# Kernel optimization log

Measured on AMD Instinct MI355X. Metric: run time of the kernel, lower is better.

## Reference

```python
import jax, jax.numpy as jnp
import numpy as np
import math

DIM = 256; SEQ = 2048; BSZ = 32; NI = 128; NS = 4; ITERS = 3

def _ln(x, g, b):
    m = x.mean(-1, keepdims=True)
    v = ((x - m) ** 2).mean(-1, keepdims=True)
    return (x - m) / jnp.sqrt(v + 1e-5) * g + b

def _norm(x):
    # torch F.normalize: x / ||x||.clamp_min(1e-12)
    return x / jnp.clip(jnp.linalg.norm(x, axis=-1, keepdims=True), 1e-12, None)

def setup_inputs() -> dict:
    key = jax.random.key(0)
    ks = jax.random.split(key, 16)
    def w(k, shape, s=0.02):
        return jax.random.normal(k, shape, jnp.float32) * s
    return {
        'tokens': jax.random.normal(ks[0], (BSZ, SEQ, DIM), jnp.float32),
        'cls_embed': jax.random.normal(ks[1], (BSZ, DIM), jnp.float32),
        'intent_queries': jax.random.normal(ks[2], (NI, DIM), jnp.float32),
        'noise': jax.random.normal(ks[3], (NI, BSZ, NS, DIM), jnp.float32),
        'Wk': w(ks[4], (DIM, DIM)), 'bk': jnp.zeros(DIM, jnp.float32),
        'Wv': w(ks[5], (DIM, DIM)), 'bv': jnp.zeros(DIM, jnp.float32),
        'Wqs': w(ks[6], (DIM, DIM)), 'bqs': jnp.zeros(DIM, jnp.float32),
        'Wqi': w(ks[7], (DIM, DIM)), 'bqi': jnp.zeros(DIM, jnp.float32),
        'ln1_g': jnp.ones(DIM, jnp.float32), 'ln1_b': jnp.zeros(DIM, jnp.float32),
        'ln2_g': jnp.ones(DIM, jnp.float32), 'ln2_b': jnp.zeros(DIM, jnp.float32),
        'Wf1': w(ks[8], (DIM, 2 * DIM)), 'bf1': jnp.zeros(2 * DIM, jnp.float32),
        'Wf2': w(ks[9], (2 * DIM, DIM)), 'bf2': jnp.zeros(DIM, jnp.float32),
        'slot_mu': w(ks[10], (1, NS, DIM)),  # randn*0.02
        'slot_sigma': jnp.ones((1, NS, DIM), jnp.float32) * 0.1,
        'alpha': jnp.float32(1.0),
        'temperature': jnp.float32(1.0),
    }

def reference(tokens, cls_embed, intent_queries, noise, Wk, bk, Wv, bv,
              Wqs, bqs, Wqi, bqi, ln1_g, ln1_b, ln2_g, ln2_b,
              Wf1, bf1, Wf2, bf2, slot_mu, slot_sigma, alpha, temperature):
    scale = 1.0 / math.sqrt(DIM)
    # k/v are identical across the per-intent loop in the original -> compute once
    k = tokens @ Wk + bk  # [B,S,D]
    v = tokens @ Wv + bv  # [B,S,D]
    cls_n = _norm(cls_embed)  # [B,D]

    def per_intent(q, eps):  # q: [D], eps: [B,NS,D]
        qn = _norm(q)
        q_intent = (q @ Wqi + bqi)[None, None, :]  # broadcast over [B,NS,:]
        slots = slot_mu[0] + eps * slot_sigma[0]   # [B,NS,D]
        for _ in range(ITERS):
            q_slot = slots @ Wqs + bqs + q_intent
            logit = jnp.einsum('bnd,bsd->bns', q_slot, k) * scale
            attn = jax.nn.softmax(logit, axis=-1)
            upd = jnp.einsum('bns,bsd->bnd', attn, v)
            slots = _ln(slots + upd, ln1_g, ln1_b)
            h = _ln(slots, ln2_g, ln2_b)
            slots = slots + jax.nn.gelu(h @ Wf1 + bf1, approximate=False) @ Wf2 + bf2
        sn = _norm(slots)                               # [B,NS,D]
        a = jax.nn.softmax(jnp.einsum('bnd,d->bn', sn, qn), axis=-1)
        summ = jnp.einsum('bn,bnd->bd', a, slots)       # slot_summary
        fused = cls_n + alpha * _norm(summ)
        return fused @ qn                               # [B]

    scores = jax.vmap(per_intent)(intent_queries, noise)  # [NI,B]
    logits = scores.T / jnp.maximum(temperature, 1e-4)    # [B,NI]
    return logits
```

## Files before the change

### kernel.cpp

```cpp
#include <hip/hip_runtime.h>
#include <math.h>

#define BSZ 32
#define NI  128

typedef __attribute__((ext_vector_type(8))) _Float16 f16x8;
typedef __attribute__((ext_vector_type(4))) _Float16 f16x4;
typedef __attribute__((ext_vector_type(4))) float    f32x4;

#define MFMA16(a, b, c) __builtin_amdgcn_mfma_f32_16x16x32_f16((a), (b), (c), 0, 0, 0)

#define GLL(g, l) __builtin_amdgcn_global_load_lds(                          \
    (const __attribute__((address_space(1))) void*)(g),                      \
    (__attribute__((address_space(3))) void*)(l), 16, 0, 0)

#define LGKM_BAR() do {                                                      \
    asm volatile("s_waitcnt lgkmcnt(0)" ::: "memory");                       \
    __builtin_amdgcn_sched_barrier(0);                                       \
    __builtin_amdgcn_s_barrier();                                            \
    __builtin_amdgcn_sched_barrier(0); } while (0)

__device__ inline float dot4f(float4 a, float4 b) {
    return a.x * b.x + a.y * b.y + a.z * b.z + a.w * b.w;
}

__device__ inline float4* slp(float* base, int r, int c) {
    return (float4*)(base + r * 256 + ((((c) >> 2) ^ (r & 7)) << 2));
}

__device__ inline void tpose64(const float* __restrict__ src, int Csrc,
                               _Float16* __restrict__ dstT, int KT,
                               int r0, int c0, _Float16 (*tbuf)[72], int tid)
{
#pragma unroll
    for (int it = 0; it < 4; it++) {
        int idx = tid + it * 256;
        int rr = idx >> 4, c4 = idx & 15;
        float4 w = *(const float4*)(src + (size_t)(r0 + rr) * Csrc + c0 + c4 * 4);
        tbuf[c4 * 4 + 0][rr] = (_Float16)w.x;
        tbuf[c4 * 4 + 1][rr] = (_Float16)w.y;
        tbuf[c4 * 4 + 2][rr] = (_Float16)w.z;
        tbuf[c4 * 4 + 3][rr] = (_Float16)w.w;
    }
    __syncthreads();
#pragma unroll
    for (int it = 0; it < 2; it++) {
        int idx = tid + it * 256;
        int orr = idx >> 3, oc8 = idx & 7;
        int n = c0 + orr;
        size_t tile = (size_t)(n >> 4) * KT + (r0 >> 5) + (oc8 >> 2);
        *(f16x8*)(dstT + tile * 512 + (n & 15) * 32 + (oc8 & 3) * 8) = *(const f16x8*)&tbuf[orr][oc8 * 8];
    }
}

__global__ __launch_bounds__(256) void prep(
    const float* __restrict__ Wk, const float* __restrict__ Wv,
    const float* __restrict__ Wqs, const float* __restrict__ Wf1,
    const float* __restrict__ Wf2,
    const float* __restrict__ intent_q, const float* __restrict__ Wqi,
    const float* __restrict__ bqi, const float* __restrict__ bqs,
    const float* __restrict__ cls_embed,
    _Float16* __restrict__ wkT, _Float16* __restrict__ wvT,
    _Float16* __restrict__ wqsT, _Float16* __restrict__ wf1T,
    _Float16* __restrict__ wf2T,
    float* __restrict__ qint2, float* __restrict__ qn, float* __restrict__ clsn)
{
    __shared__ _Float16 tbuf[64][72];
    __shared__ float buf[256];
    __shared__ float red[4];
    const int t = threadIdx.x, blk = blockIdx.x;
    const int lane = t & 63, w = t >> 6;

    if (blk < 112) {
        if (blk < 16)       tpose64(Wk, 256, wkT, 8, (blk >> 2) * 64, (blk & 3) * 64, tbuf, t);
        else if (blk < 32)  { int tt = blk - 16; tpose64(Wv, 256, wvT, 8, (tt >> 2) * 64, (tt & 3) * 64, tbuf, t); }
        else if (blk < 48)  { int tt = blk - 32; tpose64(Wqs, 256, wqsT, 8, (tt >> 2) * 64, (tt & 3) * 64, tbuf, t); }
        else if (blk < 80)  { int tt = blk - 48; tpose64(Wf1, 512, wf1T, 8, (tt & 3) * 64, (tt >> 2) * 64, tbuf, t); }
        else                { int tt = blk - 80; tpose64(Wf2, 256, wf2T, 16, (tt >> 2) * 64, (tt & 3) * 64, tbuf, t); }
    } else if (blk < 240) {
        int i = blk - 112;
        float x = intent_q[(size_t)i * 256 + t];
        buf[t] = x;
        float ss = x * x;
#pragma unroll
        for (int m = 1; m < 64; m <<= 1) ss += __shfl_xor(ss, m, 64);
        if (lane == 0) red[w] = ss;
        __syncthreads();
        float tot = red[0] + red[1] + red[2] + red[3];
        qn[(size_t)i * 256 + t] = x / fmaxf(sqrtf(tot), 1e-12f);
        float acc = bqi[t] + bqs[t];
        for (int e = 0; e < 256; e += 4) {
            const float4 q4 = *(const float4*)&buf[e];
            acc += q4.x * Wqi[(size_t)(e + 0) * 256 + t];
            acc += q4.y * Wqi[(size_t)(e + 1) * 256 + t];
            acc += q4.z * Wqi[(size_t)(e + 2) * 256 + t];
            acc += q4.w * Wqi[(size_t)(e + 3) * 256 + t];
        }
        qint2[(size_t)i * 256 + t] = acc;
    } else {
        int b = blk - 240;
        float x = cls_embed[(size_t)b * 256 + t];
        float ss = x * x;
#pragma unroll
        for (int m = 1; m < 64; m <<= 1) ss += __shfl_xor(ss, m, 64);
        if (lane == 0) red[w] = ss;
        __syncthreads();
        float tot = red[0] + red[1] + red[2] + red[3];
        clsn[(size_t)b * 256 + t] = x / fmaxf(sqrtf(tot), 1e-12f);
    }
}

__global__ __launch_bounds__(512, 2) void kvf_k(
    const float* __restrict__ tokens,
    const _Float16* __restrict__ wkT, const _Float16* __restrict__ wvT,
    const float* __restrict__ bk, const float* __restrict__ bv,
    _Float16* __restrict__ kT, _Float16* __restrict__ vT)
{
    __shared__ __align__(16) _Float16 Sb[2][8192];

    const int t = threadIdx.x, lane = t & 63, w = t >> 6;
    const int l15 = lane & 15, quad = lane >> 4;
    const int lofs = l15 * 32 + quad * 8;
    const int lofsA = ((l15 * 4 + quad) ^ ((l15 >> 1) & 7)) * 8;
    const int bx = blockIdx.x;
    const int b = bx & 31, chunk = bx >> 5;

    f16x8 wk[2][8], wv[2][8];
#pragma unroll
    for (int j = 0; j < 2; j++)
#pragma unroll
        for (int ks = 0; ks < 8; ks++) {
            wk[j][ks] = *(const f16x8*)(wkT + ((size_t)(2 * w + j) * 8 + ks) * 512 + lofs);
            wv[j][ks] = *(const f16x8*)(wvT + ((size_t)(2 * w + j) * 8 + ks) * 512 + lofs);
        }
    f32x4 bi0 = *(const f32x4*)(bk + w * 32 + quad * 4);
    f32x4 bi1 = *(const f32x4*)(bk + w * 32 + 16 + quad * 4);
    const float bv0 = bv[(2 * w) * 16 + l15];
    const float bv1 = bv[(2 * w + 1) * 16 + l15];

    const int rr = t >> 5, d8 = t & 31;
    const float* tbase = tokens + ((size_t)b * 2048 + chunk * 256) * 256 + rr * 256 + d8 * 8;
    const int mskW = ((rr >> 1) & 7) ^ (((d8 >> 2) & 3) << 1);
    const int wofs0 = (d8 >> 2) * 512 + (((rr * 4 + (d8 & 3)) ^ mskW) * 8);
    const int wofs1 = wofs0 + 8 * 512;

    float4 pa0, pa1, pb0, pb1;

#define KVF_LOADS(P) do {                                                    \
        const float* sp_ = tbase + (size_t)(P) * 8192;                       \
        pa0 = *(const float4*)(sp_);                                         \
        pa1 = *(const float4*)(sp_ + 4);                                     \
        pb0 = *(const float4*)(sp_ + 4096);                                  \
        pb1 = *(const float4*)(sp_ + 4100);                                  \
    } while (0)

#define KVF_STAGE(BUF) do {                                                  \
        f16x8 h0, h1;                                                        \
        h0[0] = (_Float16)pa0.x; h0[1] = (_Float16)pa0.y;                    \
        h0[2] = (_Float16)pa0.z; h0[3] = (_Float16)pa0.w;                    \
        h0[4] = (_Float16)pa1.x; h0[5] = (_Float16)pa1.y;                    \
        h0[6] = (_Float16)pa1.z; h0[7] = (_Float16)pa1.w;                    \
        h1[0] = (_Float16)pb0.x; h1[1] = (_Float16)pb0.y;                    \
        h1[2] = (_Float16)pb0.z; h1[3] = (_Float16)pb0.w;                    \
        h1[4] = (_Float16)pb1.x; h1[5] = (_Float16)pb1.y;                    \
        h1[6] = (_Float16)pb1.z; h1[7] = (_Float16)pb1.w;                    \
        *(f16x8*)((BUF) + wofs0) = h0;                                       \
        *(f16x8*)((BUF) + wofs1) = h1;                                       \
    } while (0)

    KVF_LOADS(0);
    KVF_STAGE(&Sb[0][0]);
    LGKM_BAR();

    for (int p = 0; p < 8; p++) {
        if (p < 7) KVF_LOADS(p + 1);
        __builtin_amdgcn_sched_barrier(0);

        const _Float16* lb = &Sb[p & 1][0];
        const int stg0 = chunk * 16 + p * 2;
        const int sp = chunk * 8 + p;

        f16x8 a[2][8];
#pragma unroll
        for (int st = 0; st < 2; st++)
#pragma unroll
            for (int ks = 0; ks < 8; ks++)
                a[st][ks] = *(const f16x8*)(lb + (st * 8 + ks) * 512 + (lofsA ^ ((ks & 3) * 16)));

#pragma unroll
        for (int st = 0; st < 2; st++) {
            f32x4 c0 = {0.f, 0.f, 0.f, 0.f}, c1 = {0.f, 0.f, 0.f, 0.f};
#pragma unroll
            for (int ks = 0; ks < 8; ks++) {
                c0 = MFMA16(wk[0][ks], a[st][ks], c0);
                c1 = MFMA16(wk[1][ks], a[st][ks], c1);
            }
            f16x4 p0, p1;
#pragma unroll
            for (int reg = 0; reg < 4; reg++) {
                p0[reg] = (_Float16)(c0[reg] + bi0[reg]);
                p1[reg] = (_Float16)(c1[reg] + bi1[reg]);
            }
            _Float16* tp = kT + ((size_t)(b * 128 + stg0 + st) * 8 + w) * 512 + l15 * 32;
            *(f16x4*)(tp + (quad >> 1) * 8 + (quad & 1) * 4) = p0;
            *(f16x4*)(tp + (2 + (quad >> 1)) * 8 + (quad & 1) * 4) = p1;
        }

#pragma unroll
        for (int j = 0; j < 2; j++) {
            f32x4 c0 = {0.f, 0.f, 0.f, 0.f}, c1 = {0.f, 0.f, 0.f, 0.f};
#pragma unroll
            for (int ks = 0; ks < 8; ks++) {
                c0 = MFMA16(a[0][ks], wv[j][ks], c0);
                c1 = MFMA16(a[1][ks], wv[j][ks], c1);
            }
            const float bb = j ? bv1 : bv0;
            f16x4 p0, p1;
#pragma unroll
            for (int reg = 0; reg < 4; reg++) {
                p0[reg] = (_Float16)(c0[reg] + bb);
                p1[reg] = (_Float16)(c1[reg] + bb);
            }
            _Float16* tp = vT + ((size_t)(b * 16 + 2 * w + j) * 64 + sp) * 512 + l15 * 32;
            *(f16x4*)(tp + (quad >> 1) * 8 + (quad & 1) * 4) = p0;
            *(f16x4*)(tp + (2 + (quad >> 1)) * 8 + (quad & 1) * 4) = p1;
        }

        if (p < 7) {
            KVF_STAGE(&Sb[(p + 1) & 1][0]);
            LGKM_BAR();
        }
    }
#undef KVF_LOADS
#undef KVF_STAGE
}

__global__ __launch_bounds__(256) void slots_init(
    const float* __restrict__ noise, const float* __restrict__ slot_mu,
    const float* __restrict__ slot_sigma, float* __restrict__ slots,
    _Float16* __restrict__ slotsT)
{
    int idx = blockIdx.x * 256 + threadIdx.x;
    int row = idx >> 5, d8 = idx & 31;
    int b = row >> 9, i = (row >> 2) & 127, n = row & 3;
    int d = d8 * 8;
    const float* mp = slot_mu + n * 256 + d;
    const float* sp = slot_sigma + n * 256 + d;
    const float* np = noise + (((size_t)i * BSZ + b) * 4 + n) * 256 + d;
    float4 o0, o1;
    {
        float4 mu = *(const float4*)mp, sg = *(const float4*)sp, ns = *(const float4*)np;
        o0.x = mu.x + ns.x * sg.x; o0.y = mu.y + ns.y * sg.y;
        o0.z = mu.z + ns.z * sg.z; o0.w = mu.w + ns.w * sg.w;
    }
    {
        float4 mu = *(const float4*)(mp + 4), sg = *(const float4*)(sp + 4), ns = *(const float4*)(np + 4);
        o1.x = mu.x + ns.x * sg.x; o1.y = mu.y + ns.y * sg.y;
        o1.z = mu.z + ns.z * sg.z; o1.w = mu.w + ns.w * sg.w;
    }
    *(float4*)(slots + (size_t)row * 256 + d) = o0;
    *(float4*)(slots + (size_t)row * 256 + d + 4) = o1;
    f16x8 h;
    h[0] = (_Float16)o0.x; h[1] = (_Float16)o0.y; h[2] = (_Float16)o0.z; h[3] = (_Float16)o0.w;
    h[4] = (_Float16)o1.x; h[5] = (_Float16)o1.y; h[6] = (_Float16)o1.z; h[7] = (_Float16)o1.w;
    *(f16x8*)(slotsT + ((size_t)(row >> 4) * 8 + (d8 >> 2)) * 512 + (row & 15) * 32 + (d8 & 3) * 8) = h;
}

__global__ __launch_bounds__(256) void qslot_k(
    const _Float16* __restrict__ slotsT, const _Float16* __restrict__ wqsT,
    const float* __restrict__ qint2, _Float16* __restrict__ qsT)
{
    const int tid = threadIdx.x, lane = tid & 63, wv = tid >> 6;
    const int l15 = lane & 15, quad = lane >> 4;
    const int lofs = l15 * 32 + quad * 8;
    const int bx = blockIdx.x, rb = bx >> 2, dq = bx & 3;
    const int rt = rb * 4 + wv;
    const int gr0 = rt * 16;

    f16x8 bs[8];
#pragma unroll
    for (int ks = 0; ks < 8; ks++)
        bs[ks] = *(const f16x8*)(slotsT + ((size_t)rt * 8 + ks) * 512 + lofs);
    const int iq = ((gr0 + l15) & 511) >> 2;
#pragma unroll
    for (int dt = 0; dt < 4; dt++) {
        int dti = dq * 4 + dt;
        f32x4 c = {0.f, 0.f, 0.f, 0.f};
#pragma unroll
        for (int ks = 0; ks < 8; ks++)
            c = MFMA16(*(const f16x8*)(wqsT + ((size_t)dti * 8 + ks) * 512 + lofs), bs[ks], c);
        float4 qi = *(const float4*)(qint2 + (size_t)iq * 256 + dti * 16 + quad * 4);
        f16x4 o;
#pragma unroll
        for (int reg = 0; reg < 4; reg++) o[reg] = (_Float16)((c[reg] + qi[reg]) * 0.0625f);
        *(f16x4*)(qsT + ((size_t)rt * 8 + (dti >> 1)) * 512 + l15 * 32
                  + ((dti & 1) * 2 + (quad >> 1)) * 8 + (quad & 1) * 4) = o;
    }
}

__global__ __launch_bounds__(512, 2) void attn_k(
    const _Float16* __restrict__ qsT, const _Float16* __restrict__ kT,
    const _Float16* __restrict__ vT,
    _Float16* __restrict__ Opart, float* __restrict__ psum4)
{
    __shared__ __align__(16) _Float16 Kb[2][16384];
    __shared__ __align__(16) _Float16 Vb[16384];
    __shared__ __align__(16) _Float16 pb[8][2304];

    const int tid = threadIdx.x, lane = tid & 63, wv = tid >> 6;
    const int l15 = lane & 15, quad = lane >> 4;
    const int lofs = l15 * 32 + quad * 8;
    const int lofsA = ((l15 * 4 + quad) ^ ((l15 >> 1) & 7)) * 8;
    const int lnsw = (lane ^ ((lane >> 3) & 7)) * 8;
    const int bx = blockIdx.x;
    const int b = bx & 31, rb = (bx >> 5) & 1, sk = bx >> 6;
    const int gr0 = b * 512 + rb * 256 + wv * 32;
    const int rt_q = gr0 >> 4;

    _Float16* pw = pb[wv];

    const _Float16* kSrc = kT + ((size_t)(b * 128 + sk * 32) * 8) * 512;

    {
        const _Float16* src = kSrc + (size_t)(wv * 4) * 512 + lnsw;
        _Float16* dst = &Kb[0][(wv * 4) * 512 + lane * 8];
#pragma unroll
        for (int j = 0; j < 4; j++) GLL(src + j * 512, dst + j * 512);
    }

    f16x8 q[2][8];
#pragma unroll
    for (int m = 0; m < 2; m++)
#pragma unroll
        for (int ks = 0; ks < 8; ks++)
            q[m][ks] = *(const f16x8*)(qsT + ((size_t)(rt_q + m) * 8 + ks) * 512 + lofs);

    f32x4 O[2][16];
#pragma unroll
    for (int m = 0; m < 2; m++)
#pragma unroll
        for (int dt = 0; dt < 16; dt++) O[m][dt] = (f32x4){0.f, 0.f, 0.f, 0.f};
    float ps[2][4] = {{0.f, 0.f, 0.f, 0.f}, {0.f, 0.f, 0.f, 0.f}};

    asm volatile("s_waitcnt vmcnt(0)" ::: "memory");
    __builtin_amdgcn_s_barrier();
    __builtin_amdgcn_sched_barrier(0);

    for (int s = 0; s < 8; s++) {
        const int cur = s & 1;

        {
            const int seg0 = wv * 4;
#pragma unroll
            for (int j = 0; j < 4; j++) {
                const int seg = seg0 + j;
                const _Float16* src = vT
                    + ((size_t)(b * 16 + (seg >> 1)) * 64 + sk * 16 + s * 2 + (seg & 1)) * 512
                    + lnsw;
                GLL(src, &Vb[seg * 512 + lane * 8]);
            }
        }
        if (s < 7) {
            const _Float16* src = kSrc + (size_t)(s + 1) * 16384 + (wv * 4) * 512 + lnsw;
            _Float16* dst = &Kb[cur ^ 1][(wv * 4) * 512 + lane * 8];
#pragma unroll
            for (int j = 0; j < 4; j++) GLL(src + j * 512, dst + j * 512);
            asm volatile("s_waitcnt vmcnt(8)" ::: "memory");
        } else {
            asm volatile("s_waitcnt vmcnt(4)" ::: "memory");
        }
        __builtin_amdgcn_s_barrier();
        __builtin_amdgcn_sched_barrier(0);

#pragma unroll
        for (int kt = 0; kt < 4; kt++) {
            const _Float16* kp = &Kb[cur][(kt * 8) * 512];
            f32x4 c0 = {0.f, 0.f, 0.f, 0.f}, c1 = {0.f, 0.f, 0.f, 0.f};
#pragma unroll
            for (int ks = 0; ks < 8; ks++) {
                f16x8 kf = *(const f16x8*)(kp + ks * 512 + lofsA);
                c0 = MFMA16(q[0][ks], kf, c0);
                c1 = MFMA16(q[1][ks], kf, c1);
            }
            const int col = kt * 16 + l15;
#pragma unroll
            for (int reg = 0; reg < 4; reg++) {
                float p0 = __expf(fminf(c0[reg], 10.5f));
                float p1 = __expf(fminf(c1[reg], 10.5f));
                ps[0][reg] += p0;
                ps[1][reg] += p1;
                pw[(quad * 4 + reg) * 72 + col] = (_Float16)p0;
                pw[(16 + quad * 4 + reg) * 72 + col] = (_Float16)p1;
            }
        }

        __builtin_amdgcn_sched_barrier(0);
        if (s < 7) {
            asm volatile("s_waitcnt vmcnt(4)" ::: "memory");
        } else {
            asm volatile("s_waitcnt vmcnt(0)" ::: "memory");
        }
        __builtin_amdgcn_s_barrier();
        __builtin_amdgcn_sched_barrier(0);

        f16x8 pa[2][2];
#pragma unroll
        for (int m = 0; m < 2; m++)
#pragma unroll
            for (int kg = 0; kg < 2; kg++)
                pa[m][kg] = *(const f16x8*)(pw + (m * 16 + l15) * 72 + kg * 32 + quad * 8);
#pragma unroll
        for (int dt = 0; dt < 16; dt++) {
            const _Float16* vp = &Vb[dt * 1024];
            f16x8 v0 = *(const f16x8*)(vp + lofsA);
            f16x8 v1 = *(const f16x8*)(vp + 512 + lofsA);
            O[0][dt] = MFMA16(pa[0][0], v0, O[0][dt]);
            O[0][dt] = MFMA16(pa[0][1], v1, O[0][dt]);
            O[1][dt] = MFMA16(pa[1][0], v0, O[1][dt]);
            O[1][dt] = MFMA16(pa[1][1], v1, O[1][dt]);
        }

        __builtin_amdgcn_sched_barrier(0);
        __builtin_amdgcn_s_barrier();
        __builtin_amdgcn_sched_barrier(0);
    }

#pragma unroll
    for (int m = 0; m < 2; m++) {
#pragma unroll
        for (int msk = 1; msk <= 8; msk <<= 1)
#pragma unroll
            for (int reg = 0; reg < 4; reg++) ps[m][reg] += __shfl_xor(ps[m][reg], msk, 64);
        if (l15 == 0) {
#pragma unroll
            for (int reg = 0; reg < 4; reg++)
                psum4[(size_t)sk * 16384 + gr0 + m * 16 + quad * 4 + reg] = ps[m][reg];
        }
    }

#pragma unroll
    for (int m = 0; m < 2; m++) {
#pragma unroll
        for (int hd = 0; hd < 2; hd++) {
#pragma unroll
            for (int dt = 0; dt < 8; dt++) {
                const int dti = hd * 8 + dt;
#pragma unroll
                for (int reg = 0; reg < 4; reg++)
                    pw[(quad * 4 + reg) * 136 + dt * 16 + l15] = (_Float16)O[m][dti][reg];
            }
#pragma unroll
            for (int p2 = 0; p2 < 4; p2++) {
                const int u = lane + p2 * 64;
                const int row = u >> 4, col8 = u & 15;
                *(f16x8*)(Opart + ((size_t)sk * 16384 + gr0 + m * 16 + row) * 256 + hd * 128 + col8 * 8) =
                    *(const f16x8*)(pw + row * 136 + col8 * 8);
            }
        }
    }
}

__global__ __launch_bounds__(256, 2) void mlp_k(
    const _Float16* __restrict__ Opart, const float* __restrict__ psum4,
    float* __restrict__ slots,
    const float* __restrict__ ln1_g, const float* __restrict__ ln1_b,
    const float* __restrict__ ln2_g, const float* __restrict__ ln2_b,
    const _Float16* __restrict__ wf1T, const float* __restrict__ bf1,
    const _Float16* __restrict__ wf2T, const float* __restrict__ bf2,
    const _Float16* __restrict__ wqsT, const float* __restrict__ qint2,
    _Float16* __restrict__ qsT,
    const float* __restrict__ qn, const float* __restrict__ clsn,
    const float* __restrict__ alphap, const float* __restrict__ tempp,
    float* __restrict__ out, int it)
{
    __shared__ float sl[32 * 256];
    __shared__ float2 st2[32];
    __shared__ __align__(16) _Float16 actL[16384];

    const int tid = threadIdx.x, lane = tid & 63, w4 = tid >> 6;
    const int l15 = lane & 15, quad = lane >> 4;
    const int lofs = l15 * 32 + quad * 8;
    const int lofsA = ((l15 * 4 + quad) ^ ((l15 >> 1) & 7)) * 8;
    const int pairW = w4 >> 1, half = w4 & 1;
    const int bx = blockIdx.x;
    const int b = bx & 31, rg = bx >> 5;
    const int R0 = b * 512 + rg * 32;

#pragma unroll
    for (int r2 = 0; r2 < 2; r2++) {
        const int lr = w4 * 8 + r2 * 4 + quad;
        const int gr = R0 + lr;
        float l = 0.f;
#pragma unroll
        for (int j = 0; j < 4; j++) l += psum4[(size_t)j * 16384 + gr];
        const float invl = 1.f / l;
        float4 y[4];
        float sm = 0.f, sq = 0.f;
#pragma unroll
        for (int k = 0; k < 4; k++) {
            const int c = k * 64 + l15 * 4;
            float4 o4 = {0.f, 0.f, 0.f, 0.f};
#pragma unroll
            for (int j = 0; j < 4; j++) {
                f16x4 p = *(const f16x4*)(Opart + ((size_t)j * 16384 + gr) * 256 + c);
                o4.x += (float)p[0]; o4.y += (float)p[1];
                o4.z += (float)p[2]; o4.w += (float)p[3];
            }
            float4 s4 = *(const float4*)(slots + (size_t)gr * 256 + c);
            y[k].x = s4.x + o4.x * invl; y[k].y = s4.y + o4.y * invl;
            y[k].z = s4.z + o4.z * invl; y[k].w = s4.w + o4.w * invl;
            sm += y[k].x + y[k].y + y[k].z + y[k].w;
            sq += dot4f(y[k], y[k]);
        }
#pragma unroll
        for (int m = 1; m <= 8; m <<= 1) { sm += __shfl_xor(sm, m, 64); sq += __shfl_xor(sq, m, 64); }
        const float mean = sm * (1.f / 256.f);
        const float rstd = rsqrtf(sq * (1.f / 256.f) - mean * mean + 1e-5f);
        float sm2 = 0.f, sq2 = 0.f;
#pragma unroll
        for (int k = 0; k < 4; k++) {
            const int c = k * 64 + l15 * 4;
            float4 g1 = *(const float4*)(ln1_g + c);
            float4 b1 = *(const float4*)(ln1_b + c);
            float4 x1;
            x1.x = (y[k].x - mean) * rstd * g1.x + b1.x;
            x1.y = (y[k].y - mean) * rstd * g1.y + b1.y;
            x1.z = (y[k].z - mean) * rstd * g1.z + b1.z;
            x1.w = (y[k].w - mean) * rstd * g1.w + b1.w;
            *slp(sl, lr, c) = x1;
            sm2 += x1.x + x1.y + x1.z + x1.w;
            sq2 += dot4f(x1, x1);
        }
#pragma unroll
        for (int m = 1; m <= 8; m <<= 1) { sm2 += __shfl_xor(sm2, m, 64); sq2 += __shfl_xor(sq2, m, 64); }
        const float mean2 = sm2 * (1.f / 256.f);
        const float rstd2 = rsqrtf(sq2 * (1.f / 256.f) - mean2 * mean2 + 1e-5f);
        if (l15 == 0) st2[lr] = make_float2(mean2, rstd2);
    }
    __syncthreads();

    const int lrf = pairW * 16 + l15;
    {
        const float2 s2 = st2[lrf];
        f16x8 bh[8];
#pragma unroll
        for (int ks = 0; ks < 8; ks++) {
            const int c0 = ks * 32 + quad * 8;
            float4 xa = *slp(sl, lrf, c0);
            float4 xb = *slp(sl, lrf, c0 + 4);
            float4 ga = *(const float4*)(ln2_g + c0);
            float4 gb = *(const float4*)(ln2_g + c0 + 4);
            float4 ba = *(const float4*)(ln2_b + c0);
            float4 bb2 = *(const float4*)(ln2_b + c0 + 4);
            bh[ks][0] = (_Float16)((xa.x - s2.x) * s2.y * ga.x + ba.x);
            bh[ks][1] = (_Float16)((xa.y - s2.x) * s2.y * ga.y + ba.y);
            bh[ks][2] = (_Float16)((xa.z - s2.x) * s2.y * ga.z + ba.z);
            bh[ks][3] = (_Float16)((xa.w - s2.x) * s2.y * ga.w + ba.w);
            bh[ks][4] = (_Float16)((xb.x - s2.x) * s2.y * gb.x + bb2.x);
            bh[ks][5] = (_Float16)((xb.y - s2.x) * s2.y * gb.y + bb2.y);
            bh[ks][6] = (_Float16)((xb.z - s2.x) * s2.y * gb.z + bb2.z);
            bh[ks][7] = (_Float16)((xb.w - s2.x) * s2.y * gb.w + bb2.w);
        }
#pragma unroll 2
        for (int t16 = 0; t16 < 16; t16++) {
            const int hti = half * 16 + t16;
            f32x4 c = {0.f, 0.f, 0.f, 0.f};
#pragma unroll
            for (int ks = 0; ks < 8; ks++)
                c = MFMA16(*(const f16x8*)(wf1T + ((size_t)hti * 8 + ks) * 512 + lofs), bh[ks], c);
            float4 bb = *(const float4*)(bf1 + hti * 16 + quad * 4);
            f16x4 o;
#pragma unroll
            for (int reg = 0; reg < 4; reg++) {
                float xg = c[reg] + bb[reg];
                o[reg] = (_Float16)(0.5f * xg * (1.f + erff(xg * 0.70710678118654752f)));
            }
            const int gA = l15 * 4 + (hti & 1) * 2 + (quad >> 1);
            *(f16x4*)(actL + ((size_t)(pairW * 16 + (hti >> 1))) * 512
                      + ((gA ^ ((l15 >> 1) & 7)) * 8) + (quad & 1) * 4) = o;
        }
    }
    __syncthreads();

    {
        f32x4 c[8];
#pragma unroll
        for (int d = 0; d < 8; d++) {
            const int dti = half * 8 + d;
            float4 x4 = *slp(sl, lrf, dti * 16 + quad * 4);
            float4 bb = *(const float4*)(bf2 + dti * 16 + quad * 4);
            c[d] = (f32x4){x4.x + bb.x, x4.y + bb.y, x4.z + bb.z, x4.w + bb.w};
        }
        const _Float16* ap = actL + ((size_t)pairW * 16) * 512;
        for (int ks = 0; ks < 16; ks++) {
            f16x8 afrag = *(const f16x8*)(ap + (size_t)ks * 512 + lofsA);
#pragma unroll
            for (int d = 0; d < 8; d++)
                c[d] = MFMA16(*(const f16x8*)(wf2T + ((size_t)(half * 8 + d) * 16 + ks) * 512 + lofs),
                              afrag, c[d]);
        }
#pragma unroll
        for (int d = 0; d < 8; d++) {
            const int dti = half * 8 + d;
            float4 v = {c[d][0], c[d][1], c[d][2], c[d][3]};
            *slp(sl, lrf, dti * 16 + quad * 4) = v;
        }
    }
    __syncthreads();

    if (it < 2) {
        f16x8 bs[8];
#pragma unroll
        for (int ks = 0; ks < 8; ks++) {
            const int c0 = ks * 32 + quad * 8;
            float4 xa = *slp(sl, lrf, c0);
            float4 xb = *slp(sl, lrf, c0 + 4);
            bs[ks][0] = (_Float16)xa.x; bs[ks][1] = (_Float16)xa.y;
            bs[ks][2] = (_Float16)xa.z; bs[ks][3] = (_Float16)xa.w;
            bs[ks][4] = (_Float16)xb.x; bs[ks][5] = (_Float16)xb.y;
            bs[ks][6] = (_Float16)xb.z; bs[ks][7] = (_Float16)xb.w;
        }
        const int iq = (rg * 32 + pairW * 16 + l15) >> 2;
        const int rtg = b * 32 + rg * 2 + pairW;
#pragma unroll
        for (int d = 0; d < 8; d++) {
            const int dti = half * 8 + d;
            f32x4 c = {0.f, 0.f, 0.f, 0.f};
#pragma unroll
            for (int ks = 0; ks < 8; ks++)
                c = MFMA16(*(const f16x8*)(wqsT + ((size_t)dti * 8 + ks) * 512 + lofs), bs[ks], c);
            float4 qi = *(const float4*)(qint2 + (size_t)iq * 256 + dti * 16 + quad * 4);
            f16x4 o;
#pragma unroll
            for (int reg = 0; reg < 4; reg++) o[reg] = (_Float16)((c[reg] + qi[reg]) * 0.0625f);
            *(f16x4*)(qsT + ((size_t)rtg * 8 + (dti >> 1)) * 512 + l15 * 32
                      + ((dti & 1) * 2 + (quad >> 1)) * 8 + (quad & 1) * 4) = o;
        }
        {
            const int lr2 = tid >> 3, k8 = tid & 7;
#pragma unroll
            for (int q4 = 0; q4 < 8; q4++) {
                float4 v = *slp(sl, lr2, k8 * 32 + q4 * 4);
                *(float4*)(slots + (size_t)(R0 + lr2) * 256 + k8 * 32 + q4 * 4) = v;
            }
        }
    } else {
#pragma unroll
        for (int ii = 0; ii < 2; ii++) {
            const int i_loc = w4 * 2 + ii;
            const int i = rg * 8 + i_loc;
            float4 qv = *(const float4*)(qn + (size_t)i * 256 + lane * 4);
            float4 xs[4];
            float st4[4];
#pragma unroll
            for (int n = 0; n < 4; n++) {
                xs[n] = *slp(sl, i_loc * 4 + n, lane * 4);
                float ss = dot4f(xs[n], xs[n]);
                float sq = dot4f(xs[n], qv);
#pragma unroll
                for (int m = 1; m < 64; m <<= 1) { ss += __shfl_xor(ss, m, 64); sq += __shfl_xor(sq, m, 64); }
                st4[n] = sq / fmaxf(sqrtf(ss), 1e-12f);
            }
            float mx = fmaxf(fmaxf(st4[0], st4[1]), fmaxf(st4[2], st4[3]));
            float e0 = __expf(st4[0] - mx), e1 = __expf(st4[1] - mx);
            float e2 = __expf(st4[2] - mx), e3 = __expf(st4[3] - mx);
            float inv = 1.f / (e0 + e1 + e2 + e3);
            float4 smv;
            smv.x = (e0 * xs[0].x + e1 * xs[1].x + e2 * xs[2].x + e3 * xs[3].x) * inv;
            smv.y = (e0 * xs[0].y + e1 * xs[1].y + e2 * xs[2].y + e3 * xs[3].y) * inv;
            smv.z = (e0 * xs[0].z + e1 * xs[1].z + e2 * xs[2].z + e3 * xs[3].z) * inv;
            smv.w = (e0 * xs[0].w + e1 * xs[1].w + e2 * xs[2].w + e3 * xs[3].w) * inv;
            float ssm = dot4f(smv, smv);
            float sqn = dot4f(smv, qv);
            float4 cv = *(const float4*)(clsn + (size_t)b * 256 + lane * 4);
            float cq = dot4f(cv, qv);
#pragma unroll
            for (int m = 1; m < 64; m <<= 1) {
                ssm += __shfl_xor(ssm, m, 64);
                sqn += __shfl_xor(sqn, m, 64);
                cq  += __shfl_xor(cq,  m, 64);
            }
            if (lane == 0) {
                float score = cq + alphap[0] * sqn / fmaxf(sqrtf(ssm), 1e-12f);
                out[(size_t)b * NI + i] = score / fmaxf(tempp[0], 1e-4f);
            }
        }
    }
}

extern "C" void kernel_launch(void* const* d_in, const int* in_sizes, int n_in,
                              void* d_out, int out_size, void* d_ws, size_t ws_size,
                              hipStream_t stream)
{
    const float* tokens     = (const float*)d_in[0];
    const float* cls_embed  = (const float*)d_in[1];
    const float* intent_q   = (const float*)d_in[2];
    const float* noise      = (const float*)d_in[3];
    const float* Wk  = (const float*)d_in[4];
    const float* bk  = (const float*)d_in[5];
    const float* Wv  = (const float*)d_in[6];
    const float* bv  = (const float*)d_in[7];
    const float* Wqs = (const float*)d_in[8];
    const float* bqs = (const float*)d_in[9];
    const float* Wqi = (const float*)d_in[10];
    const float* bqi = (const float*)d_in[11];
    const float* ln1g = (const float*)d_in[12];
    const float* ln1b = (const float*)d_in[13];
    const float* ln2g = (const float*)d_in[14];
    const float* ln2b = (const float*)d_in[15];
    const float* Wf1 = (const float*)d_in[16];
    const float* bf1 = (const float*)d_in[17];
    const float* Wf2 = (const float*)d_in[18];
    const float* bf2 = (const float*)d_in[19];
    const float* slot_mu    = (const float*)d_in[20];
    const float* slot_sigma = (const float*)d_in[21];
    const float* alphap = (const float*)d_in[22];
    const float* tempp  = (const float*)d_in[23];
    float* out = (float*)d_out;

    char* base = (char*)d_ws;
    _Float16* qsT   = (_Float16*)(base);
    _Float16* slotsT= (_Float16*)(base + 8388608u);
    _Float16* kT    = (_Float16*)(base + 33554432u);
    _Float16* vT    = (_Float16*)(base + 67108864u);
    _Float16* Opart = (_Float16*)(base + 100663296u);
    float* slots    = (float*)(base + 134217728u);
    _Float16* wkT   = (_Float16*)(base + 150994944u);
    _Float16* wvT   = (_Float16*)(base + 151126016u);
    _Float16* wqsT  = (_Float16*)(base + 151257088u);
    _Float16* wf1T  = (_Float16*)(base + 151388160u);
    _Float16* wf2T  = (_Float16*)(base + 151650304u);
    float* qint2    = (float*)(base + 151912448u);
    float* qnb      = (float*)(base + 152043520u);
    float* clsn     = (float*)(base + 152174592u);
    float* psum4    = (float*)(base + 152207360u);

    prep<<<272, 256, 0, stream>>>(Wk, Wv, Wqs, Wf1, Wf2, intent_q, Wqi, bqi, bqs,
                                  cls_embed, wkT, wvT, wqsT, wf1T, wf2T,
                                  qint2, qnb, clsn);
    kvf_k<<<256, 512, 0, stream>>>(tokens, wkT, wvT, bk, bv, kT, vT);
    slots_init<<<2048, 256, 0, stream>>>(noise, slot_mu, slot_sigma, slots, slotsT);
    qslot_k<<<1024, 256, 0, stream>>>(slotsT, wqsT, qint2, qsT);

    for (int it = 0; it < 3; it++) {
        attn_k<<<256, 512, 0, stream>>>(qsT, kT, vT, Opart, psum4);
        mlp_k<<<512, 256, 0, stream>>>(Opart, psum4, slots,
                                       ln1g, ln1b, ln2g, ln2b,
                                       wf1T, bf1, wf2T, bf2,
                                       wqsT, qint2, qsT,
                                       qnb, clsn, alphap, tempp, out, it);
    }
}
```

Measured before the change: 490.0 us.

## Fuse slot init with q-slot projection and halve mlp_k rows per block

Merges slots_init and qslot_k into one kernel that builds the slot rows in shared memory and projects them with Wqs directly, which drops the fp16 slotsT round trip and one launch. mlp_k now handles 16 rows per block instead of 32, with the grid doubled to 1024 and occupancy raised to 4 blocks per CU. Shared memory per block is halved and each wave covers a quarter of the output columns instead of pairs of waves splitting the work. Each block now reloads the Wf1/Wf2/Wqs weight fragments for fewer rows, so weight traffic per row goes up. An extra barrier guards the in-place writes to shared memory.

Measured after the change: 473.6 us. -3.3%, faster.

```diff
diff --git a/kernel.cpp b/kernel.cpp
--- a/kernel.cpp
+++ b/kernel.cpp
@@ -235,56 +235,54 @@
 #undef KVF_STAGE
 }
 
-__global__ __launch_bounds__(256) void slots_init(
+__global__ __launch_bounds__(256, 4) void slotq_k(
     const float* __restrict__ noise, const float* __restrict__ slot_mu,
-    const float* __restrict__ slot_sigma, float* __restrict__ slots,
-    _Float16* __restrict__ slotsT)
+    const float* __restrict__ slot_sigma,
+    const _Float16* __restrict__ wqsT, const float* __restrict__ qint2,
+    float* __restrict__ slots, _Float16* __restrict__ qsT)
 {
-    int idx = blockIdx.x * 256 + threadIdx.x;
-    int row = idx >> 5, d8 = idx & 31;
-    int b = row >> 9, i = (row >> 2) & 127, n = row & 3;
-    int d = d8 * 8;
-    const float* mp = slot_mu + n * 256 + d;
-    const float* sp = slot_sigma + n * 256 + d;
-    const float* np = noise + (((size_t)i * BSZ + b) * 4 + n) * 256 + d;
-    float4 o0, o1;
-    {
-        float4 mu = *(const float4*)mp, sg = *(const float4*)sp, ns = *(const float4*)np;
-        o0.x = mu.x + ns.x * sg.x; o0.y = mu.y + ns.y * sg.y;
-        o0.z = mu.z + ns.z * sg.z; o0.w = mu.w + ns.w * sg.w;
-    }
-    {
-        float4 mu = *(const float4*)(mp + 4), sg = *(const float4*)(sp + 4), ns = *(const float4*)(np + 4);
-        o1.x = mu.x + ns.x * sg.x; o1.y = mu.y + ns.y * sg.y;
-        o1.z = mu.z + ns.z * sg.z; o1.w = mu.w + ns.w * sg.w;
-    }
-    *(float4*)(slots + (size_t)row * 256 + d) = o0;
-    *(float4*)(slots + (size_t)row * 256 + d + 4) = o1;
-    f16x8 h;
-    h[0] = (_Float16)o0.x; h[1] = (_Float16)o0.y; h[2] = (_Float16)o0.z; h[3] = (_Float16)o0.w;
-    h[4] = (_Float16)o1.x; h[5] = (_Float16)o1.y; h[6] = (_Float16)o1.z; h[7] = (_Float16)o1.w;
-    *(f16x8*)(slotsT + ((size_t)(row >> 4) * 8 + (d8 >> 2)) * 512 + (row & 15) * 32 + (d8 & 3) * 8) = h;
-}
-
-__global__ __launch_bounds__(256) void qslot_k(
-    const _Float16* __restrict__ slotsT, const _Float16* __restrict__ wqsT,
-    const float* __restrict__ qint2, _Float16* __restrict__ qsT)
-{
-    const int tid = threadIdx.x, lane = tid & 63, wv = tid >> 6;
+    __shared__ float sb[16 * 256];
+    const int tid = threadIdx.x, lane = tid & 63, w4 = tid >> 6;
     const int l15 = lane & 15, quad = lane >> 4;
     const int lofs = l15 * 32 + quad * 8;
-    const int bx = blockIdx.x, rb = bx >> 2, dq = bx & 3;
-    const int rt = rb * 4 + wv;
+    const int rt = blockIdx.x;
     const int gr0 = rt * 16;
 
+    {
+        const int lr = w4 * 4 + quad;
+        const int gr = gr0 + lr;
+        const int b = gr >> 9, i = (gr >> 2) & 127, n = gr & 3;
+        const float* np = noise + (((size_t)i * BSZ + b) * 4 + n) * 256;
+#pragma unroll
+        for (int k = 0; k < 4; k++) {
+            const int c = k * 64 + l15 * 4;
+            float4 mu = *(const float4*)(slot_mu + n * 256 + c);
+            float4 sg = *(const float4*)(slot_sigma + n * 256 + c);
+            float4 ns = *(const float4*)(np + c);
+            float4 o;
+            o.x = mu.x + ns.x * sg.x; o.y = mu.y + ns.y * sg.y;
+            o.z = mu.z + ns.z * sg.z; o.w = mu.w + ns.w * sg.w;
+            *slp(sb, lr, c) = o;
+            *(float4*)(slots + (size_t)gr * 256 + c) = o;
+        }
+    }
+    __syncthreads();
+
     f16x8 bs[8];
 #pragma unroll
-    for (int ks = 0; ks < 8; ks++)
-        bs[ks] = *(const f16x8*)(slotsT + ((size_t)rt * 8 + ks) * 512 + lofs);
+    for (int ks = 0; ks < 8; ks++) {
+        const int c0 = ks * 32 + quad * 8;
+        float4 xa = *slp(sb, l15, c0);
+        float4 xb = *slp(sb, l15, c0 + 4);
+        bs[ks][0] = (_Float16)xa.x; bs[ks][1] = (_Float16)xa.y;
+        bs[ks][2] = (_Float16)xa.z; bs[ks][3] = (_Float16)xa.w;
+        bs[ks][4] = (_Float16)xb.x; bs[ks][5] = (_Float16)xb.y;
+        bs[ks][6] = (_Float16)xb.z; bs[ks][7] = (_Float16)xb.w;
+    }
     const int iq = ((gr0 + l15) & 511) >> 2;
 #pragma unroll
-    for (int dt = 0; dt < 4; dt++) {
-        int dti = dq * 4 + dt;
+    for (int d = 0; d < 4; d++) {
+        const int dti = w4 * 4 + d;
         f32x4 c = {0.f, 0.f, 0.f, 0.f};
 #pragma unroll
         for (int ks = 0; ks < 8; ks++)
@@ -460,7 +458,7 @@
     }
 }
 
-__global__ __launch_bounds__(256, 2) void mlp_k(
+__global__ __launch_bounds__(256, 4) void mlp_k(
     const _Float16* __restrict__ Opart, const float* __restrict__ psum4,
     float* __restrict__ slots,
     const float* __restrict__ ln1_g, const float* __restrict__ ln1_b,
@@ -473,22 +471,20 @@
     const float* __restrict__ alphap, const float* __restrict__ tempp,
     float* __restrict__ out, int it)
 {
-    __shared__ float sl[32 * 256];
-    __shared__ float2 st2[32];
-    __shared__ __align__(16) _Float16 actL[16384];
+    __shared__ float sl[16 * 256];
+    __shared__ float2 st2[16];
+    __shared__ __align__(16) _Float16 actL[8192];
 
     const int tid = threadIdx.x, lane = tid & 63, w4 = tid >> 6;
     const int l15 = lane & 15, quad = lane >> 4;
     const int lofs = l15 * 32 + quad * 8;
     const int lofsA = ((l15 * 4 + quad) ^ ((l15 >> 1) & 7)) * 8;
-    const int pairW = w4 >> 1, half = w4 & 1;
     const int bx = blockIdx.x;
     const int b = bx & 31, rg = bx >> 5;
-    const int R0 = b * 512 + rg * 32;
-
-#pragma unroll
-    for (int r2 = 0; r2 < 2; r2++) {
-        const int lr = w4 * 8 + r2 * 4 + quad;
+    const int R0 = b * 512 + rg * 16;
+
+    {
+        const int lr = w4 * 4 + quad;
         const int gr = R0 + lr;
         float l = 0.f;
 #pragma unroll
@@ -539,15 +535,14 @@
     }
     __syncthreads();
 
-    const int lrf = pairW * 16 + l15;
     {
-        const float2 s2 = st2[lrf];
+        const float2 s2 = st2[l15];
         f16x8 bh[8];
 #pragma unroll
         for (int ks = 0; ks < 8; ks++) {
             const int c0 = ks * 32 + quad * 8;
-            float4 xa = *slp(sl, lrf, c0);
-            float4 xb = *slp(sl, lrf, c0 + 4);
+            float4 xa = *slp(sl, l15, c0);
+            float4 xb = *slp(sl, l15, c0 + 4);
             float4 ga = *(const float4*)(ln2_g + c0);
             float4 gb = *(const float4*)(ln2_g + c0 + 4);
             float4 ba = *(const float4*)(ln2_b + c0);
@@ -562,8 +557,8 @@
             bh[ks][7] = (_Float16)((xb.w - s2.x) * s2.y * gb.w + bb2.w);
         }
 #pragma unroll 2
-        for (int t16 = 0; t16 < 16; t16++) {
-            const int hti = half * 16 + t16;
+        for (int t8 = 0; t8 < 8; t8++) {
+            const int hti = w4 * 8 + t8;
             f32x4 c = {0.f, 0.f, 0.f, 0.f};
 #pragma unroll
             for (int ks = 0; ks < 8; ks++)
@@ -576,34 +571,34 @@
                 o[reg] = (_Float16)(0.5f * xg * (1.f + erff(xg * 0.70710678118654752f)));
             }
             const int gA = l15 * 4 + (hti & 1) * 2 + (quad >> 1);
-            *(f16x4*)(actL + ((size_t)(pairW * 16 + (hti >> 1))) * 512
+            *(f16x4*)(actL + ((size_t)(hti >> 1)) * 512
                       + ((gA ^ ((l15 >> 1) & 7)) * 8) + (quad & 1) * 4) = o;
         }
     }
     __syncthreads();
 
     {
-        f32x4 c[8];
-#pragma unroll
-        for (int d = 0; d < 8; d++) {
-            const int dti = half * 8 + d;
-            float4 x4 = *slp(sl, lrf, dti * 16 + quad * 4);
+        f32x4 c[4];
+#pragma unroll
+        for (int d = 0; d < 4; d++) {
+            const int dti = w4 * 4 + d;
+            float4 x4 = *slp(sl, l15, dti * 16 + quad * 4);
             float4 bb = *(const float4*)(bf2 + dti * 16 + quad * 4);
             c[d] = (f32x4){x4.x + bb.x, x4.y + bb.y, x4.z + bb.z, x4.w + bb.w};
         }
-        const _Float16* ap = actL + ((size_t)pairW * 16) * 512;
         for (int ks = 0; ks < 16; ks++) {
-            f16x8 afrag = *(const f16x8*)(ap + (size_t)ks * 512 + lofsA);
-#pragma unroll
-            for (int d = 0; d < 8; d++)
-                c[d] = MFMA16(*(const f16x8*)(wf2T + ((size_t)(half * 8 + d) * 16 + ks) * 512 + lofs),
+            f16x8 afrag = *(const f16x8*)(actL + (size_t)ks * 512 + lofsA);
+#pragma unroll
+            for (int d = 0; d < 4; d++)
+                c[d] = MFMA16(*(const f16x8*)(wf2T + ((size_t)(w4 * 4 + d) * 16 + ks) * 512 + lofs),
                               afrag, c[d]);
         }
-#pragma unroll
-        for (int d = 0; d < 8; d++) {
-            const int dti = half * 8 + d;
+        __syncthreads();
+#pragma unroll
+        for (int d = 0; d < 4; d++) {
+            const int dti = w4 * 4 + d;
             float4 v = {c[d][0], c[d][1], c[d][2], c[d][3]};
-            *slp(sl, lrf, dti * 16 + quad * 4) = v;
+            *slp(sl, l15, dti * 16 + quad * 4) = v;
         }
     }
     __syncthreads();
@@ -613,18 +608,18 @@
 #pragma unroll
         for (int ks = 0; ks < 8; ks++) {
             const int c0 = ks * 32 + quad * 8;
-            float4 xa = *slp(sl, lrf, c0);
-            float4 xb = *slp(sl, lrf, c0 + 4);
+            float4 xa = *slp(sl, l15, c0);
+            float4 xb = *slp(sl, l15, c0 + 4);
             bs[ks][0] = (_Float16)xa.x; bs[ks][1] = (_Float16)xa.y;
             bs[ks][2] = (_Float16)xa.z; bs[ks][3] = (_Float16)xa.w;
             bs[ks][4] = (_Float16)xb.x; bs[ks][5] = (_Float16)xb.y;
             bs[ks][6] = (_Float16)xb.z; bs[ks][7] = (_Float16)xb.w;
         }
-        const int iq = (rg * 32 + pairW * 16 + l15) >> 2;
-        const int rtg = b * 32 + rg * 2 + pairW;
-#pragma unroll
-        for (int d = 0; d < 8; d++) {
-            const int dti = half * 8 + d;
+        const int iq = rg * 4 + (l15 >> 2);
+        const int rtg = b * 32 + rg;
+#pragma unroll
+        for (int d = 0; d < 4; d++) {
+            const int dti = w4 * 4 + d;
             f32x4 c = {0.f, 0.f, 0.f, 0.f};
 #pragma unroll
             for (int ks = 0; ks < 8; ks++)
@@ -637,53 +632,49 @@
                       + ((dti & 1) * 2 + (quad >> 1)) * 8 + (quad & 1) * 4) = o;
         }
         {
-            const int lr2 = tid >> 3, k8 = tid & 7;
-#pragma unroll
-            for (int q4 = 0; q4 < 8; q4++) {
-                float4 v = *slp(sl, lr2, k8 * 32 + q4 * 4);
-                *(float4*)(slots + (size_t)(R0 + lr2) * 256 + k8 * 32 + q4 * 4) = v;
+            const int lr2 = tid >> 4, c16 = tid & 15;
+#pragma unroll
+            for (int q4 = 0; q4 < 4; q4++) {
+                float4 v = *slp(sl, lr2, c16 * 16 + q4 * 4);
+                *(float4*)(slots + (size_t)(R0 + lr2) * 256 + c16 * 16 + q4 * 4) = v;
             }
         }
     } else {
-#pragma unroll
-        for (int ii = 0; ii < 2; ii++) {
-            const int i_loc = w4 * 2 + ii;
-            const int i = rg * 8 + i_loc;
-            float4 qv = *(const float4*)(qn + (size_t)i * 256 + lane * 4);
-            float4 xs[4];
-            float st4[4];
-#pragma unroll
-            for (int n = 0; n < 4; n++) {
-                xs[n] = *slp(sl, i_loc * 4 + n, lane * 4);
-                float ss = dot4f(xs[n], xs[n]);
-                float sq = dot4f(xs[n], qv);
-#pragma unroll
-                for (int m = 1; m < 64; m <<= 1) { ss += __shfl_xor(ss, m, 64); sq += __shfl_xor(sq, m, 64); }
-                st4[n] = sq / fmaxf(sqrtf(ss), 1e-12f);
-            }
-            float mx = fmaxf(fmaxf(st4[0], st4[1]), fmaxf(st4[2], st4[3]));
-            float e0 = __expf(st4[0] - mx), e1 = __expf(st4[1] - mx);
-            float e2 = __expf(st4[2] - mx), e3 = __expf(st4[3] - mx);
-            float inv = 1.f / (e0 + e1 + e2 + e3);
-            float4 smv;
-            smv.x = (e0 * xs[0].x + e1 * xs[1].x + e2 * xs[2].x + e3 * xs[3].x) * inv;
-            smv.y = (e0 * xs[0].y + e1 * xs[1].y + e2 * xs[2].y + e3 * xs[3].y) * inv;
-            smv.z = (e0 * xs[0].z + e1 * xs[1].z + e2 * xs[2].z + e3 * xs[3].z) * inv;
-            smv.w = (e0 * xs[0].w + e1 * xs[1].w + e2 * xs[2].w + e3 * xs[3].w) * inv;
-            float ssm = dot4f(smv, smv);
-            float sqn = dot4f(smv, qv);
-            float4 cv = *(const float4*)(clsn + (size_t)b * 256 + lane * 4);
-            float cq = dot4f(cv, qv);
-#pragma unroll
-            for (int m = 1; m < 64; m <<= 1) {
-                ssm += __shfl_xor(ssm, m, 64);
-                sqn += __shfl_xor(sqn, m, 64);
-                cq  += __shfl_xor(cq,  m, 64);
-            }
-            if (lane == 0) {
-                float score = cq + alphap[0] * sqn / fmaxf(sqrtf(ssm), 1e-12f);
-                out[(size_t)b * NI + i] = score / fmaxf(tempp[0], 1e-4f);
-            }
+        const int i = rg * 4 + w4;
+        float4 qv = *(const float4*)(qn + (size_t)i * 256 + lane * 4);
+        float4 xs[4];
+        float st4[4];
+#pragma unroll
+        for (int n = 0; n < 4; n++) {
+            xs[n] = *slp(sl, w4 * 4 + n, lane * 4);
+            float ss = dot4f(xs[n], xs[n]);
+            float sq = dot4f(xs[n], qv);
+#pragma unroll
+            for (int m = 1; m < 64; m <<= 1) { ss += __shfl_xor(ss, m, 64); sq += __shfl_xor(sq, m, 64); }
+            st4[n] = sq / fmaxf(sqrtf(ss), 1e-12f);
+        }
+        float mx = fmaxf(fmaxf(st4[0], st4[1]), fmaxf(st4[2], st4[3]));
+        float e0 = __expf(st4[0] - mx), e1 = __expf(st4[1] - mx);
+        float e2 = __expf(st4[2] - mx), e3 = __expf(st4[3] - mx);
+        float inv = 1.f / (e0 + e1 + e2 + e3);
+        float4 smv;
+        smv.x = (e0 * xs[0].x + e1 * xs[1].x + e2 * xs[2].x + e3 * xs[3].x) * inv;
+        smv.y = (e0 * xs[0].y + e1 * xs[1].y + e2 * xs[2].y + e3 * xs[3].y) * inv;
+        smv.z = (e0 * xs[0].z + e1 * xs[1].z + e2 * xs[2].z + e3 * xs[3].z) * inv;
+        smv.w = (e0 * xs[0].w + e1 * xs[1].w + e2 * xs[2].w + e3 * xs[3].w) * inv;
+        float ssm = dot4f(smv, smv);
+        float sqn = dot4f(smv, qv);
+        float4 cv = *(const float4*)(clsn + (size_t)b * 256 + lane * 4);
+        float cq = dot4f(cv, qv);
+#pragma unroll
+        for (int m = 1; m < 64; m <<= 1) {
+            ssm += __shfl_xor(ssm, m, 64);
+            sqn += __shfl_xor(sqn, m, 64);
+            cq  += __shfl_xor(cq,  m, 64);
+        }
+        if (lane == 0) {
+            float score = cq + alphap[0] * sqn / fmaxf(sqrtf(ssm), 1e-12f);
+            out[(size_t)b * NI + i] = score / fmaxf(tempp[0], 1e-4f);
         }
     }
 }
@@ -720,7 +711,6 @@
 
     char* base = (char*)d_ws;
     _Float16* qsT   = (_Float16*)(base);
-    _Float16* slotsT= (_Float16*)(base + 8388608u);
     _Float16* kT    = (_Float16*)(base + 33554432u);
     _Float16* vT    = (_Float16*)(base + 67108864u);
     _Float16* Opart = (_Float16*)(base + 100663296u);
@@ -739,15 +729,15 @@
                                   cls_embed, wkT, wvT, wqsT, wf1T, wf2T,
                                   qint2, qnb, clsn);
     kvf_k<<<256, 512, 0, stream>>>(tokens, wkT, wvT, bk, bv, kT, vT);
-    slots_init<<<2048, 256, 0, stream>>>(noise, slot_mu, slot_sigma, slots, slotsT);
-    qslot_k<<<1024, 256, 0, stream>>>(slotsT, wqsT, qint2, qsT);
+    slotq_k<<<1024, 256, 0, stream>>>(noise, slot_mu, slot_sigma, wqsT, qint2,
+                                      slots, qsT);
 
     for (int it = 0; it < 3; it++) {
         attn_k<<<256, 512, 0, stream>>>(qsT, kT, vT, Opart, psum4);
-        mlp_k<<<512, 256, 0, stream>>>(Opart, psum4, slots,
-                                       ln1g, ln1b, ln2g, ln2b,
-                                       wf1T, bf1, wf2T, bf2,
-                                       wqsT, qint2, qsT,
-                                       qnb, clsn, alphap, tempp, out, it);
-    }
-}
+        mlp_k<<<1024, 256, 0, stream>>>(Opart, psum4, slots,
+                                        ln1g, ln1b, ln2g, ln2b,
+                                        wf1T, bf1, wf2T, bf2,
+                                        wqsT, qint2, qsT,
+                                        qnb, clsn, alphap, tempp, out, it);
+    }
+}
```
